# Kernel optimization log

Hardware: AMD Instinct MI355X
Metric: run time of the kernel (lower is better)

The kernel has to match this reference:

```python
import jax, jax.numpy as jnp
import numpy as np

EPS = 1e-5
THRESH = 0.05
NUM_THINGS = 3
D = 256
EGO_PC_RANGE = np.array([-51.2, -51.2, -5.0, 51.2, 51.2, 3.0], np.float32)


def _inverse_sigmoid(x):
    x = jnp.clip(x, 0.0, 1.0)
    return jnp.log(jnp.maximum(x, EPS) / jnp.maximum(1.0 - x, EPS))


def setup_inputs() -> dict:
    key = jax.random.key(0)
    ks = jax.random.split(key, 16)
    L, B, Qo, Qv = 6, 1, 8192, 8192
    # class logits uniform in [0,1) -> sigmoid >= 0.5 > threshold, so all queries pass (deterministic shapes)
    other_outputs_classes = jax.random.uniform(ks[0], (L, B, Qo, NUM_THINGS), jnp.float32)
    other_outputs_coords = jax.random.uniform(ks[1], (L, B, Qo, 4), jnp.float32)
    other_query = jax.random.normal(ks[2], (B, Qo, D), jnp.float32)
    other_query_pos = jax.random.normal(ks[3], (B, Qo, D), jnp.float32)
    other_reference = jax.random.normal(ks[4], (B, Qo, 4), jnp.float32)
    veh_outputs_classes = jax.random.normal(ks[5], (L, B, Qv, NUM_THINGS), jnp.float32)
    veh_outputs_coords = jax.random.uniform(ks[6], (L, B, Qv, 4), jnp.float32)
    veh_query = jax.random.normal(ks[7], (B, Qv, D), jnp.float32)
    veh_query_pos = jax.random.normal(ks[8], (B, Qv, D), jnp.float32)
    veh_reference = jax.random.normal(ks[9], (B, Qv, 4), jnp.float32)
    # rigid ego->other transform (rotation about z + translation), invertible by construction
    th = 0.3
    rt = np.eye(4, dtype=np.float32)
    rt[0, 0] = np.cos(th); rt[0, 1] = -np.sin(th)
    rt[1, 0] = np.sin(th); rt[1, 1] = np.cos(th)
    rt[0, 3] = 12.0; rt[1, 3] = -5.0; rt[2, 3] = 0.3
    ego2other_rt = jnp.asarray(rt)[None]  # [1,4,4]
    other_agent_pc_range = jnp.asarray(EGO_PC_RANGE)
    xav = float(np.sqrt(2.0 / (D + 9 + D)))
    Wa = jax.random.normal(ks[10], (D + 9, D), jnp.float32) * xav
    ba = jax.random.normal(ks[11], (D,), jnp.float32) * 0.01
    Wp = jax.random.normal(ks[12], (D + 9, D), jnp.float32) * xav
    bp = jax.random.normal(ks[13], (D,), jnp.float32) * 0.01
    return dict(other_outputs_classes=other_outputs_classes, other_outputs_coords=other_outputs_coords,
                other_query=other_query, other_query_pos=other_query_pos, other_reference=other_reference,
                veh_outputs_classes=veh_outputs_classes, veh_outputs_coords=veh_outputs_coords,
                veh_query=veh_query, veh_query_pos=veh_query_pos, veh_reference=veh_reference,
                ego2other_rt=ego2other_rt, other_agent_pc_range=other_agent_pc_range,
                Wa=Wa, ba=ba, Wp=Wp, bp=bp)


def reference(other_outputs_classes, other_outputs_coords, other_query, other_query_pos, other_reference,
              veh_outputs_classes, veh_outputs_coords, veh_query, veh_query_pos, veh_reference,
              ego2other_rt, other_agent_pc_range, Wa, ba, Wp, bp):
    calib = jnp.linalg.inv(ego2other_rt[0].T)  # other -> ego, [4,4]
    # filter_other_lanes (eager: concrete inputs, data-dependent selection like torch.where)
    cls = jax.nn.sigmoid(other_outputs_classes[-1])
    bbox_index = jnp.where(cls.reshape(-1) > THRESH)[0] // NUM_THINGS
    ooc_cls = other_outputs_classes[:, :, bbox_index]      # [L,B,N,3]
    ooc = other_outputs_coords[:, :, bbox_index]           # [L,B,N,4]
    oq = other_query[:, bbox_index]                        # [B,N,D]
    oqp = other_query_pos[:, bbox_index]
    oref = other_reference[:, bbox_index]                  # [B,N,4]
    lo, hi = other_agent_pc_range[:3], other_agent_pc_range[3:]
    elo = jnp.asarray(EGO_PC_RANGE[:3]); ehi = jnp.asarray(EGO_PC_RANGE[3:])
    # --- reference points: inverse_sigmoid space, z logit = 0 ---
    p = jax.nn.sigmoid(jnp.concatenate([oref[..., :2], jnp.zeros_like(oref[..., :1])], -1))
    p = p * (hi - lo) + lo                                 # other lidar coords
    h = jnp.concatenate([p, jnp.ones_like(p[..., :1])], -1)
    p = jnp.einsum('ij,bnj->bni', calib, h)[..., :3]       # ego lidar coords
    p = _inverse_sigmoid((p - elo) / (ehi - elo))
    oref = jnp.concatenate([p[..., :2], oref[..., 2:]], -1)
    # --- bbox centers: already sigmoided, z norm = 0 ---
    b = jnp.concatenate([ooc[..., :2], jnp.zeros_like(ooc[..., :1])], -1)
    b = b * (hi - lo) + lo
    hb = jnp.concatenate([b, jnp.ones_like(b[..., :1])], -1)
    b = jnp.einsum('ij,lbnj->lbni', calib, hb)[..., :3]
    b = (b - elo) / (ehi - elo)
    ooc = jnp.concatenate([b[..., :2], ooc[..., 2:]], -1)
    # --- cross-agent query alignment: concat flattened 3x3 rotation, small Linear ---
    r9 = jnp.broadcast_to(calib[:3, :3].reshape(9), oq.shape[:2] + (9,))
    oq = jnp.concatenate([oq, r9], -1) @ Wa + ba
    oqp = jnp.concatenate([oqp, r9], -1) @ Wp + bp
    return (jnp.concatenate([veh_outputs_classes, ooc_cls], axis=2),
            jnp.concatenate([veh_outputs_coords, ooc], axis=2),
            jnp.concatenate([veh_query, oq], axis=1),
            jnp.concatenate([veh_query_pos, oqp], axis=1),
            jnp.concatenate([veh_reference, oref], axis=1))
```

## Files before the change

kernel.cpp:

```cpp
#include <hip/hip_runtime.h>
#include <stdint.h>

typedef float f32x4 __attribute__((ext_vector_type(4)));
typedef __bf16 bf16x8 __attribute__((ext_vector_type(8)));
typedef __bf16 bf16x4 __attribute__((ext_vector_type(4)));

namespace {
constexpr int L = 6, Qo = 8192, Qv = 8192, NT = 3, D = 256;
constexpr int ROWS = Qv + 3 * Qo;
constexpr int OUT0 = 0;
constexpr int OUT1 = L * ROWS * NT;
constexpr int OUT2 = OUT1 + L * ROWS * 4;
constexpr int OUT3 = OUT2 + ROWS * D;
constexpr int OUT4 = OUT3 + ROWS * D;
constexpr float ELO0 = -51.2f, ELO1 = -51.2f, EHI0 = 51.2f, EHI1 = 51.2f;
constexpr int NB_GEMM = 512;
constexpr int NB_STREAM = 1536;
constexpr int NB_TOT = NB_GEMM + NB_STREAM;
constexpr int R_COPY = 2 * Qv * D / 4;
constexpr int R_OUT1 = R_COPY + L * ROWS;
constexpr int R_OUT4 = R_OUT1 + ROWS;
constexpr int R_TOT  = R_OUT4 + L * ROWS * NT / 4;
}

__device__ __forceinline__ float sigmoidf(float x) { return 1.f / (1.f + __expf(-x)); }
__device__ __forceinline__ float invsig(float v) {
    float x = fminf(fmaxf(v, 0.f), 1.f);
    return __logf(fmaxf(x, 1e-5f) / fmaxf(1.f - x, 1e-5f));
}

__device__ void inv4x4_T(const float* __restrict__ rt, float* __restrict__ C) {
    float m[16], inv[16];
    for (int i = 0; i < 4; i++)
        for (int j = 0; j < 4; j++) m[i * 4 + j] = rt[j * 4 + i];
    inv[0]  =  m[5]*m[10]*m[15] - m[5]*m[11]*m[14] - m[9]*m[6]*m[15] + m[9]*m[7]*m[14] + m[13]*m[6]*m[11] - m[13]*m[7]*m[10];
    inv[4]  = -m[4]*m[10]*m[15] + m[4]*m[11]*m[14] + m[8]*m[6]*m[15] - m[8]*m[7]*m[14] - m[12]*m[6]*m[11] + m[12]*m[7]*m[10];
    inv[8]  =  m[4]*m[9]*m[15]  - m[4]*m[11]*m[13] - m[8]*m[5]*m[15] + m[8]*m[7]*m[13] + m[12]*m[5]*m[11] - m[12]*m[7]*m[9];
    inv[12] = -m[4]*m[9]*m[14]  + m[4]*m[10]*m[13] + m[8]*m[5]*m[14] - m[8]*m[6]*m[13] - m[12]*m[5]*m[10] + m[12]*m[6]*m[9];
    inv[1]  = -m[1]*m[10]*m[15] + m[1]*m[11]*m[14] + m[9]*m[2]*m[15] - m[9]*m[3]*m[14] - m[13]*m[2]*m[11] + m[13]*m[3]*m[10];
    inv[5]  =  m[0]*m[10]*m[15] - m[0]*m[11]*m[14] - m[8]*m[2]*m[15] + m[8]*m[3]*m[14] + m[12]*m[2]*m[11] - m[12]*m[3]*m[10];
    inv[9]  = -m[0]*m[9]*m[15]  + m[0]*m[11]*m[13] + m[8]*m[1]*m[15] - m[8]*m[3]*m[13] - m[12]*m[1]*m[11] + m[12]*m[3]*m[9];
    inv[13] =  m[0]*m[9]*m[14]  - m[0]*m[10]*m[13] - m[8]*m[1]*m[14] + m[8]*m[2]*m[13] + m[12]*m[1]*m[10] - m[12]*m[2]*m[9];
    inv[2]  =  m[1]*m[6]*m[15]  - m[1]*m[7]*m[14]  - m[5]*m[2]*m[15] + m[5]*m[3]*m[14] + m[13]*m[2]*m[7]  - m[13]*m[3]*m[6];
    inv[6]  = -m[0]*m[6]*m[15]  + m[0]*m[7]*m[14]  + m[4]*m[2]*m[15] - m[4]*m[3]*m[14] - m[12]*m[2]*m[7]  + m[12]*m[3]*m[6];
    inv[10] =  m[0]*m[5]*m[15]  - m[0]*m[7]*m[13]  - m[4]*m[1]*m[15] + m[4]*m[3]*m[13] + m[12]*m[1]*m[7]  - m[12]*m[3]*m[5];
    inv[14] = -m[0]*m[5]*m[14]  + m[0]*m[6]*m[13]  + m[4]*m[1]*m[14] - m[4]*m[2]*m[13] - m[12]*m[1]*m[6]  + m[12]*m[2]*m[5];
    inv[3]  = -m[1]*m[6]*m[11]  + m[1]*m[7]*m[10]  + m[5]*m[2]*m[11] - m[5]*m[3]*m[10] - m[9]*m[2]*m[7]   + m[9]*m[3]*m[6];
    inv[7]  =  m[0]*m[6]*m[11]  - m[0]*m[7]*m[10]  - m[4]*m[2]*m[11] + m[4]*m[3]*m[10] + m[8]*m[2]*m[7]   - m[8]*m[3]*m[6];
    inv[11] = -m[0]*m[5]*m[11]  + m[0]*m[7]*m[9]   + m[4]*m[1]*m[11] - m[4]*m[3]*m[9]  - m[8]*m[1]*m[7]   + m[8]*m[3]*m[5];
    inv[15] =  m[0]*m[5]*m[10]  - m[0]*m[6]*m[9]   - m[4]*m[1]*m[10] + m[4]*m[2]*m[9]  + m[8]*m[1]*m[6]   - m[8]*m[2]*m[5];
    float det = m[0]*inv[0] + m[1]*inv[4] + m[2]*inv[8] + m[3]*inv[12];
    det = 1.0f / det;
    for (int i = 0; i < 16; i++) C[i] = inv[i] * det;
}

__global__ __launch_bounds__(256, 8) void fused(
    const float* __restrict__ ocls, const float* __restrict__ ocoord,
    const float* __restrict__ oq, const float* __restrict__ oqp,
    const float* __restrict__ oref, const float* __restrict__ vcls,
    const float* __restrict__ vcoord, const float* __restrict__ vq,
    const float* __restrict__ vqp, const float* __restrict__ vref,
    const float* __restrict__ rt, const float* __restrict__ pcr,
    const float* __restrict__ Wa, const float* __restrict__ ba,
    const float* __restrict__ Wp, const float* __restrict__ bp,
    float* __restrict__ out) {
    __shared__ __attribute__((aligned(16))) char lds[16576];
    float* ldsBias  = (float*)&lds[16384];
    float* ldsCalib = (float*)&lds[16512];
    const int b = blockIdx.x;
    const int t = threadIdx.x;

    if (b < NB_GEMM) {
        const int r = b & 7, ny = (b >> 3) & 7, s = b >> 6;
        const int u = s * 8 + r, which = u >> 5, mg = u & 31;
        const float* Asrc = which ? oqp : oq;
        const float* Wsrc = which ? Wp : Wa;
        const float* bv   = which ? bp : ba;
        const size_t obase = which ? (size_t)OUT3 : (size_t)OUT2;
        const int n0 = ny * 32;
        if (t == 0) inv4x4_T(rt, ldsCalib);
        {
            int kloc = t >> 3;
            int n4 = (t & 7) * 4;
            #pragma unroll
            for (int pass = 0; pass < 8; ++pass) {
                int k = pass * 32 + kloc;
                f32x4 v = *(const f32x4*)&Wsrc[(size_t)k * D + n0 + n4];
                #pragma unroll
                for (int i = 0; i < 4; ++i) {
                    int n = n4 + i;
                    *(__bf16*)&lds[n * 512 + ((2 * k) ^ ((n & 7) << 4))] = (__bf16)v[i];
                }
            }
        }
        __syncthreads();
        if (t < 32) {
            float sum = bv[n0 + t];
            #pragma unroll
            for (int m2 = 0; m2 < 9; m2++)
                sum += ldsCalib[(m2 / 3) * 4 + (m2 % 3)] * Wsrc[(size_t)(D + m2) * D + n0 + t];
            ldsBias[t] = sum;
        }
        __syncthreads();
        const int lane = t & 63, wave = t >> 6, lrow = lane & 15, grp = lane >> 4;
        #pragma unroll
        for (int mi = 0; mi < 4; ++mi) {
            const int am = (mg * 4 + mi) * 64 + wave * 16 + lrow;
            const float* Ap = Asrc + (size_t)am * D;
            f32x4 acc[2] = {f32x4{0,0,0,0}, f32x4{0,0,0,0}};
            #pragma unroll
            for (int ks = 0; ks < 8; ++ks) {
                f32x4 a0 = *(const f32x4*)&Ap[ks * 32 + grp * 8];
                f32x4 a1 = *(const f32x4*)&Ap[ks * 32 + grp * 8 + 4];
                bf16x8 af = {(__bf16)a0.x, (__bf16)a0.y, (__bf16)a0.z, (__bf16)a0.w,
                             (__bf16)a1.x, (__bf16)a1.y, (__bf16)a1.z, (__bf16)a1.w};
                int kb = ks * 64 + grp * 16;
                #pragma unroll
                for (int nt = 0; nt < 2; ++nt) {
                    int c = nt * 16 + lrow;
                    bf16x8 w = *(const bf16x8*)&lds[c * 512 + (kb ^ ((c & 7) << 4))];
                    acc[nt] = __builtin_amdgcn_mfma_f32_16x16x32_bf16(w, af, acc[nt], 0, 0, 0);
                }
            }
            size_t rbase = obase + (size_t)(Qv + 3 * am) * D + n0;
            #pragma unroll
            for (int nt = 0; nt < 2; ++nt) {
                f32x4 bz = *(const f32x4*)&ldsBias[nt * 16 + grp * 4];
                f32x4 v = acc[nt] + bz;
                float* p = out + rbase + nt * 16 + grp * 4;
                *(f32x4*)p = v;
                *(f32x4*)(p + D) = v;
                *(f32x4*)(p + 2 * D) = v;
            }
        }
        return;
    }

    if (t == 0) inv4x4_T(rt, ldsCalib);
    __syncthreads();
    const float c00 = ldsCalib[0], c01 = ldsCalib[1], c02 = ldsCalib[2], c03 = ldsCalib[3];
    const float c10 = ldsCalib[4], c11 = ldsCalib[5], c12 = ldsCalib[6], c13 = ldsCalib[7];
    const float lo0 = pcr[0], lo1 = pcr[1], lo2 = pcr[2];
    const float hi0 = pcr[3], hi1 = pcr[4], hi2 = pcr[5];
    const int stride = NB_STREAM * 256;
    for (int c = (b - NB_GEMM) * 256 + t; c < R_TOT; c += stride) {
        if (c < R_COPY) {
            const int HALF = Qv * D / 4;
            const float* src = (c < HALF) ? vq : vqp;
            size_t ob = (c < HALF) ? (size_t)OUT2 : (size_t)OUT3;
            int j = (c < HALF) ? c : c - HALF;
            *(f32x4*)&out[ob + (size_t)j * 4] = *(const f32x4*)&src[(size_t)j * 4];
        } else if (c < R_OUT1) {
            int tid = c - R_COPY;
            unsigned l = (unsigned)tid >> 15, rr = (unsigned)tid & 32767u;
            f32x4 o;
            if (rr < (unsigned)Qv) {
                o = *(const f32x4*)&vcoord[((size_t)l * Qv + rr) * 4];
            } else {
                unsigned q = (rr - Qv) / 3u;
                f32x4 s = *(const f32x4*)&ocoord[((size_t)l * Qo + q) * 4];
                float bx = s.x * (hi0 - lo0) + lo0;
                float by = s.y * (hi1 - lo1) + lo1;
                float bz = lo2;
                float px = c00 * bx + c01 * by + c02 * bz + c03;
                float py = c10 * bx + c11 * by + c12 * bz + c13;
                o.x = (px - ELO0) / (EHI0 - ELO0);
                o.y = (py - ELO1) / (EHI1 - ELO1);
                o.z = s.z; o.w = s.w;
            }
            *(f32x4*)&out[OUT1 + (size_t)tid * 4] = o;
        } else if (c < R_OUT4) {
            unsigned rr = (unsigned)(c - R_OUT1);
            f32x4 o;
            if (rr < (unsigned)Qv) {
                o = *(const f32x4*)&vref[(size_t)rr * 4];
            } else {
                unsigned q = (rr - Qv) / 3u;
                f32x4 s = *(const f32x4*)&oref[(size_t)q * 4];
                float bx = sigmoidf(s.x) * (hi0 - lo0) + lo0;
                float by = sigmoidf(s.y) * (hi1 - lo1) + lo1;
                float bz = 0.5f * (hi2 - lo2) + lo2;
                float px = c00 * bx + c01 * by + c02 * bz + c03;
                float py = c10 * bx + c11 * by + c12 * bz + c13;
                o.x = invsig((px - ELO0) / (EHI0 - ELO0));
                o.y = invsig((py - ELO1) / (EHI1 - ELO1));
                o.z = s.z; o.w = s.w;
            }
            *(f32x4*)&out[OUT4 + (size_t)rr * 4] = o;
        } else {
            int e0 = (c - R_OUT4) * 4;
            f32x4 o;
            #pragma unroll
            for (int i = 0; i < 4; ++i) {
                unsigned e = (unsigned)(e0 + i);
                unsigned l = e / (unsigned)(ROWS * NT);
                unsigned rem = e - l * (ROWS * NT);
                unsigned rr = rem / 3u;
                float v;
                if (rr < (unsigned)Qv) v = vcls[l * (Qv * NT) + rem];
                else {
                    unsigned cc = rem - rr * 3u;
                    unsigned q = (rr - Qv) / 3u;
                    v = ocls[l * (Qo * NT) + q * 3u + cc];
                }
                o[i] = v;
            }
            *(f32x4*)&out[OUT0 + (size_t)e0] = o;
        }
    }
}

extern "C" void kernel_launch(void* const* d_in, const int* in_sizes, int n_in,
                              void* d_out, int out_size, void* d_ws, size_t ws_size,
                              hipStream_t stream) {
    const float* ocls   = (const float*)d_in[0];
    const float* ocoord = (const float*)d_in[1];
    const float* oq     = (const float*)d_in[2];
    const float* oqp    = (const float*)d_in[3];
    const float* oref   = (const float*)d_in[4];
    const float* vcls   = (const float*)d_in[5];
    const float* vcoord = (const float*)d_in[6];
    const float* vq     = (const float*)d_in[7];
    const float* vqp    = (const float*)d_in[8];
    const float* vref   = (const float*)d_in[9];
    const float* rt     = (const float*)d_in[10];
    const float* pcr    = (const float*)d_in[11];
    const float* Wa     = (const float*)d_in[12];
    const float* ba     = (const float*)d_in[13];
    const float* Wp     = (const float*)d_in[14];
    const float* bp     = (const float*)d_in[15];
    float* out = (float*)d_out;

    hipLaunchKernelGGL(fused, dim3(NB_TOT), dim3(256), 0, stream,
                       ocls, ocoord, oq, oqp, oref, vcls, vcoord, vq, vqp, vref,
                       rt, pcr, Wa, ba, Wp, bp, out);
}
```

Measured before the change: 30.89 us.

## Split fused kernel into separate GEMM and streaming-copy launches with finer work split

Replaces the single fused kernel, which gave GEMM blocks and grid-strided stream blocks role-based work, with two kernels. The GEMM kernel now launches 2048 blocks that each handle one 64-row M tile instead of four. The stream kernel uses a fixed, non-strided mapping of 1024 vec4 elements per block, with separate block ranges for the plain copies, the coord/ref transforms and the class gather. The aim is better load balance and fewer branches per thread, at the cost of a second launch and no overlap between GEMM and streaming work. Each GEMM block also redoes the weight-tile staging and matrix inverse for less work.

```diff
diff --git a/kernel.cpp b/kernel.cpp
--- a/kernel.cpp
+++ b/kernel.cpp
@@ -14,13 +14,13 @@
 constexpr int OUT3 = OUT2 + ROWS * D;
 constexpr int OUT4 = OUT3 + ROWS * D;
 constexpr float ELO0 = -51.2f, ELO1 = -51.2f, EHI0 = 51.2f, EHI1 = 51.2f;
-constexpr int NB_GEMM = 512;
-constexpr int NB_STREAM = 1536;
-constexpr int NB_TOT = NB_GEMM + NB_STREAM;
+constexpr int NB_GEMM = 2048;
 constexpr int R_COPY = 2 * Qv * D / 4;
 constexpr int R_OUT1 = R_COPY + L * ROWS;
 constexpr int R_OUT4 = R_OUT1 + ROWS;
 constexpr int R_TOT  = R_OUT4 + L * ROWS * NT / 4;
+constexpr int NB_STREAM = R_TOT / 1024;
+constexpr int HALF = Qv * D / 4;
 }
 
 __device__ __forceinline__ float sigmoidf(float x) { return 1.f / (1.f + __expf(-x)); }
@@ -54,159 +54,171 @@
     for (int i = 0; i < 16; i++) C[i] = inv[i] * det;
 }
 
-__global__ __launch_bounds__(256, 8) void fused(
+__global__ __launch_bounds__(256, 8) void k_gemm(
+    const float* __restrict__ oq, const float* __restrict__ oqp,
+    const float* __restrict__ Wa, const float* __restrict__ ba,
+    const float* __restrict__ Wp, const float* __restrict__ bp,
+    const float* __restrict__ rt, float* __restrict__ out) {
+    __shared__ __attribute__((aligned(16))) char lds[16576];
+    float* ldsBias  = (float*)&lds[16384];
+    float* ldsCalib = (float*)&lds[16512];
+    const int b = blockIdx.x, t = threadIdx.x;
+    const int ny = b >> 8, mg = (b & 255) >> 1, which = b & 1;
+    const float* Asrc = which ? oqp : oq;
+    const float* Wsrc = which ? Wp : Wa;
+    const float* bv   = which ? bp : ba;
+    const size_t obase = which ? (size_t)OUT3 : (size_t)OUT2;
+    const int n0 = ny * 32;
+    if (t == 0) inv4x4_T(rt, ldsCalib);
+    {
+        int kloc = t >> 3;
+        int n4 = (t & 7) * 4;
+        #pragma unroll
+        for (int pass = 0; pass < 8; ++pass) {
+            int k = pass * 32 + kloc;
+            f32x4 v = *(const f32x4*)&Wsrc[(size_t)k * D + n0 + n4];
+            #pragma unroll
+            for (int i = 0; i < 4; ++i) {
+                int n = n4 + i;
+                *(__bf16*)&lds[n * 512 + ((2 * k) ^ ((n & 7) << 4))] = (__bf16)v[i];
+            }
+        }
+    }
+    __syncthreads();
+    if (t < 32) {
+        float sum = bv[n0 + t];
+        #pragma unroll
+        for (int m2 = 0; m2 < 9; m2++)
+            sum += ldsCalib[(m2 / 3) * 4 + (m2 % 3)] * Wsrc[(size_t)(D + m2) * D + n0 + t];
+        ldsBias[t] = sum;
+    }
+    __syncthreads();
+    const int lane = t & 63, wave = t >> 6, lrow = lane & 15, grp = lane >> 4;
+    const int am = mg * 64 + wave * 16 + lrow;
+    const float* Ap = Asrc + (size_t)am * D;
+    f32x4 acc[2] = {f32x4{0,0,0,0}, f32x4{0,0,0,0}};
+    #pragma unroll
+    for (int ks = 0; ks < 8; ++ks) {
+        f32x4 a0 = *(const f32x4*)&Ap[ks * 32 + grp * 8];
+        f32x4 a1 = *(const f32x4*)&Ap[ks * 32 + grp * 8 + 4];
+        bf16x8 af = {(__bf16)a0.x, (__bf16)a0.y, (__bf16)a0.z, (__bf16)a0.w,
+                     (__bf16)a1.x, (__bf16)a1.y, (__bf16)a1.z, (__bf16)a1.w};
+        int kb = ks * 64 + grp * 16;
+        #pragma unroll
+        for (int nt = 0; nt < 2; ++nt) {
+            int c = nt * 16 + lrow;
+            bf16x8 w = *(const bf16x8*)&lds[c * 512 + (kb ^ ((c & 7) << 4))];
+            acc[nt] = __builtin_amdgcn_mfma_f32_16x16x32_bf16(w, af, acc[nt], 0, 0, 0);
+        }
+    }
+    size_t rbase = obase + (size_t)(Qv + 3 * am) * D + n0;
+    #pragma unroll
+    for (int nt = 0; nt < 2; ++nt) {
+        f32x4 bz = *(const f32x4*)&ldsBias[nt * 16 + grp * 4];
+        f32x4 v = acc[nt] + bz;
+        float* p = out + rbase + nt * 16 + grp * 4;
+        *(f32x4*)p = v;
+        *(f32x4*)(p + D) = v;
+        *(f32x4*)(p + 2 * D) = v;
+    }
+}
+
+__global__ __launch_bounds__(256, 8) void k_stream(
     const float* __restrict__ ocls, const float* __restrict__ ocoord,
-    const float* __restrict__ oq, const float* __restrict__ oqp,
     const float* __restrict__ oref, const float* __restrict__ vcls,
     const float* __restrict__ vcoord, const float* __restrict__ vq,
     const float* __restrict__ vqp, const float* __restrict__ vref,
     const float* __restrict__ rt, const float* __restrict__ pcr,
-    const float* __restrict__ Wa, const float* __restrict__ ba,
-    const float* __restrict__ Wp, const float* __restrict__ bp,
     float* __restrict__ out) {
-    __shared__ __attribute__((aligned(16))) char lds[16576];
-    float* ldsBias  = (float*)&lds[16384];
-    float* ldsCalib = (float*)&lds[16512];
-    const int b = blockIdx.x;
-    const int t = threadIdx.x;
-
-    if (b < NB_GEMM) {
-        const int r = b & 7, ny = (b >> 3) & 7, s = b >> 6;
-        const int u = s * 8 + r, which = u >> 5, mg = u & 31;
-        const float* Asrc = which ? oqp : oq;
-        const float* Wsrc = which ? Wp : Wa;
-        const float* bv   = which ? bp : ba;
-        const size_t obase = which ? (size_t)OUT3 : (size_t)OUT2;
-        const int n0 = ny * 32;
+    __shared__ float ldsCalib[16];
+    const int b = blockIdx.x, t = threadIdx.x;
+
+    if (b < 1024) {
+        const float* src = (b < 512) ? vq : vqp;
+        const size_t ob = (b < 512) ? (size_t)OUT2 : (size_t)OUT3;
+        const int j0 = (b & 511) * 1024 + t;
+        f32x4 v0 = *(const f32x4*)&src[(size_t)j0 * 4];
+        f32x4 v1 = *(const f32x4*)&src[(size_t)(j0 + 256) * 4];
+        f32x4 v2 = *(const f32x4*)&src[(size_t)(j0 + 512) * 4];
+        f32x4 v3 = *(const f32x4*)&src[(size_t)(j0 + 768) * 4];
+        *(f32x4*)&out[ob + (size_t)j0 * 4] = v0;
+        *(f32x4*)&out[ob + (size_t)(j0 + 256) * 4] = v1;
+        *(f32x4*)&out[ob + (size_t)(j0 + 512) * 4] = v2;
+        *(f32x4*)&out[ob + (size_t)(j0 + 768) * 4] = v3;
+        return;
+    }
+    if (b < 1248) {
         if (t == 0) inv4x4_T(rt, ldsCalib);
-        {
-            int kloc = t >> 3;
-            int n4 = (t & 7) * 4;
-            #pragma unroll
-            for (int pass = 0; pass < 8; ++pass) {
-                int k = pass * 32 + kloc;
-                f32x4 v = *(const f32x4*)&Wsrc[(size_t)k * D + n0 + n4];
-                #pragma unroll
-                for (int i = 0; i < 4; ++i) {
-                    int n = n4 + i;
-                    *(__bf16*)&lds[n * 512 + ((2 * k) ^ ((n & 7) << 4))] = (__bf16)v[i];
+        __syncthreads();
+        const float c00 = ldsCalib[0], c01 = ldsCalib[1], c02 = ldsCalib[2], c03 = ldsCalib[3];
+        const float c10 = ldsCalib[4], c11 = ldsCalib[5], c12 = ldsCalib[6], c13 = ldsCalib[7];
+        const float lo0 = pcr[0], lo1 = pcr[1], lo2 = pcr[2];
+        const float hi0 = pcr[3], hi1 = pcr[4], hi2 = pcr[5];
+        #pragma unroll
+        for (int k = 0; k < 4; ++k) {
+            int c = b * 1024 + t + k * 256;
+            if (c < R_OUT1) {
+                int tid = c - R_COPY;
+                unsigned l = (unsigned)tid >> 15, rr = (unsigned)tid & 32767u;
+                f32x4 o;
+                if (rr < (unsigned)Qv) {
+                    o = *(const f32x4*)&vcoord[((size_t)l * Qv + rr) * 4];
+                } else {
+                    unsigned q = (rr - Qv) / 3u;
+                    f32x4 s = *(const f32x4*)&ocoord[((size_t)l * Qo + q) * 4];
+                    float bx = s.x * (hi0 - lo0) + lo0;
+                    float by = s.y * (hi1 - lo1) + lo1;
+                    float bz = lo2;
+                    float px = c00 * bx + c01 * by + c02 * bz + c03;
+                    float py = c10 * bx + c11 * by + c12 * bz + c13;
+                    o.x = (px - ELO0) / (EHI0 - ELO0);
+                    o.y = (py - ELO1) / (EHI1 - ELO1);
+                    o.z = s.z; o.w = s.w;
                 }
+                *(f32x4*)&out[OUT1 + (size_t)tid * 4] = o;
+            } else {
+                unsigned rr = (unsigned)(c - R_OUT1);
+                f32x4 o;
+                if (rr < (unsigned)Qv) {
+                    o = *(const f32x4*)&vref[(size_t)rr * 4];
+                } else {
+                    unsigned q = (rr - Qv) / 3u;
+                    f32x4 s = *(const f32x4*)&oref[(size_t)q * 4];
+                    float bx = sigmoidf(s.x) * (hi0 - lo0) + lo0;
+                    float by = sigmoidf(s.y) * (hi1 - lo1) + lo1;
+                    float bz = 0.5f * (hi2 - lo2) + lo2;
+                    float px = c00 * bx + c01 * by + c02 * bz + c03;
+                    float py = c10 * bx + c11 * by + c12 * bz + c13;
+                    o.x = invsig((px - ELO0) / (EHI0 - ELO0));
+                    o.y = invsig((py - ELO1) / (EHI1 - ELO1));
+                    o.z = s.z; o.w = s.w;
+                }
+                *(f32x4*)&out[OUT4 + (size_t)rr * 4] = o;
             }
         }
-        __syncthreads();
-        if (t < 32) {
-            float sum = bv[n0 + t];
-            #pragma unroll
-            for (int m2 = 0; m2 < 9; m2++)
-                sum += ldsCalib[(m2 / 3) * 4 + (m2 % 3)] * Wsrc[(size_t)(D + m2) * D + n0 + t];
-            ldsBias[t] = sum;
-        }
-        __syncthreads();
-        const int lane = t & 63, wave = t >> 6, lrow = lane & 15, grp = lane >> 4;
-        #pragma unroll
-        for (int mi = 0; mi < 4; ++mi) {
-            const int am = (mg * 4 + mi) * 64 + wave * 16 + lrow;
-            const float* Ap = Asrc + (size_t)am * D;
-            f32x4 acc[2] = {f32x4{0,0,0,0}, f32x4{0,0,0,0}};
-            #pragma unroll
-            for (int ks = 0; ks < 8; ++ks) {
-                f32x4 a0 = *(const f32x4*)&Ap[ks * 32 + grp * 8];
-                f32x4 a1 = *(const f32x4*)&Ap[ks * 32 + grp * 8 + 4];
-                bf16x8 af = {(__bf16)a0.x, (__bf16)a0.y, (__bf16)a0.z, (__bf16)a0.w,
-                             (__bf16)a1.x, (__bf16)a1.y, (__bf16)a1.z, (__bf16)a1.w};
-                int kb = ks * 64 + grp * 16;
-                #pragma unroll
-                for (int nt = 0; nt < 2; ++nt) {
-                    int c = nt * 16 + lrow;
-                    bf16x8 w = *(const bf16x8*)&lds[c * 512 + (kb ^ ((c & 7) << 4))];
-                    acc[nt] = __builtin_amdgcn_mfma_f32_16x16x32_bf16(w, af, acc[nt], 0, 0, 0);
-                }
+        return;
+    }
+    #pragma unroll
+    for (int k = 0; k < 4; ++k) {
+        int c = b * 1024 + t + k * 256;
+        int e0 = (c - R_OUT4) * 4;
+        f32x4 o;
+        #pragma unroll
+        for (int i = 0; i < 4; ++i) {
+            unsigned e = (unsigned)(e0 + i);
+            unsigned l = e / (unsigned)(ROWS * NT);
+            unsigned rem = e - l * (ROWS * NT);
+            unsigned rr = rem / 3u;
+            float v;
+            if (rr < (unsigned)Qv) v = vcls[l * (Qv * NT) + rem];
+            else {
+                unsigned cc = rem - rr * 3u;
+                unsigned q = (rr - Qv) / 3u;
+                v = ocls[l * (Qo * NT) + q * 3u + cc];
             }
-            size_t rbase = obase + (size_t)(Qv + 3 * am) * D + n0;
-            #pragma unroll
-            for (int nt = 0; nt < 2; ++nt) {
-                f32x4 bz = *(const f32x4*)&ldsBias[nt * 16 + grp * 4];
-                f32x4 v = acc[nt] + bz;
-                float* p = out + rbase + nt * 16 + grp * 4;
-                *(f32x4*)p = v;
-                *(f32x4*)(p + D) = v;
-                *(f32x4*)(p + 2 * D) = v;
-            }
-        }
-        return;
-    }
-
-    if (t == 0) inv4x4_T(rt, ldsCalib);
-    __syncthreads();
-    const float c00 = ldsCalib[0], c01 = ldsCalib[1], c02 = ldsCalib[2], c03 = ldsCalib[3];
-    const float c10 = ldsCalib[4], c11 = ldsCalib[5], c12 = ldsCalib[6], c13 = ldsCalib[7];
-    const float lo0 = pcr[0], lo1 = pcr[1], lo2 = pcr[2];
-    const float hi0 = pcr[3], hi1 = pcr[4], hi2 = pcr[5];
-    const int stride = NB_STREAM * 256;
-    for (int c = (b - NB_GEMM) * 256 + t; c < R_TOT; c += stride) {
-        if (c < R_COPY) {
-            const int HALF = Qv * D / 4;
-            const float* src = (c < HALF) ? vq : vqp;
-            size_t ob = (c < HALF) ? (size_t)OUT2 : (size_t)OUT3;
-            int j = (c < HALF) ? c : c - HALF;
-            *(f32x4*)&out[ob + (size_t)j * 4] = *(const f32x4*)&src[(size_t)j * 4];
-        } else if (c < R_OUT1) {
-            int tid = c - R_COPY;
-            unsigned l = (unsigned)tid >> 15, rr = (unsigned)tid & 32767u;
-            f32x4 o;
-            if (rr < (unsigned)Qv) {
-                o = *(const f32x4*)&vcoord[((size_t)l * Qv + rr) * 4];
-            } else {
-                unsigned q = (rr - Qv) / 3u;
-                f32x4 s = *(const f32x4*)&ocoord[((size_t)l * Qo + q) * 4];
-                float bx = s.x * (hi0 - lo0) + lo0;
-                float by = s.y * (hi1 - lo1) + lo1;
-                float bz = lo2;
-                float px = c00 * bx + c01 * by + c02 * bz + c03;
-                float py = c10 * bx + c11 * by + c12 * bz + c13;
-                o.x = (px - ELO0) / (EHI0 - ELO0);
-                o.y = (py - ELO1) / (EHI1 - ELO1);
-                o.z = s.z; o.w = s.w;
-            }
-            *(f32x4*)&out[OUT1 + (size_t)tid * 4] = o;
-        } else if (c < R_OUT4) {
-            unsigned rr = (unsigned)(c - R_OUT1);
-            f32x4 o;
-            if (rr < (unsigned)Qv) {
-                o = *(const f32x4*)&vref[(size_t)rr * 4];
-            } else {
-                unsigned q = (rr - Qv) / 3u;
-                f32x4 s = *(const f32x4*)&oref[(size_t)q * 4];
-                float bx = sigmoidf(s.x) * (hi0 - lo0) + lo0;
-                float by = sigmoidf(s.y) * (hi1 - lo1) + lo1;
-                float bz = 0.5f * (hi2 - lo2) + lo2;
-                float px = c00 * bx + c01 * by + c02 * bz + c03;
-                float py = c10 * bx + c11 * by + c12 * bz + c13;
-                o.x = invsig((px - ELO0) / (EHI0 - ELO0));
-                o.y = invsig((py - ELO1) / (EHI1 - ELO1));
-                o.z = s.z; o.w = s.w;
-            }
-            *(f32x4*)&out[OUT4 + (size_t)rr * 4] = o;
-        } else {
-            int e0 = (c - R_OUT4) * 4;
-            f32x4 o;
-            #pragma unroll
-            for (int i = 0; i < 4; ++i) {
-                unsigned e = (unsigned)(e0 + i);
-                unsigned l = e / (unsigned)(ROWS * NT);
-                unsigned rem = e - l * (ROWS * NT);
-                unsigned rr = rem / 3u;
-                float v;
-                if (rr < (unsigned)Qv) v = vcls[l * (Qv * NT) + rem];
-                else {
-                    unsigned cc = rem - rr * 3u;
-                    unsigned q = (rr - Qv) / 3u;
-                    v = ocls[l * (Qo * NT) + q * 3u + cc];
-                }
-                o[i] = v;
-            }
-            *(f32x4*)&out[OUT0 + (size_t)e0] = o;
-        }
+            o[i] = v;
+        }
+        *(f32x4*)&out[OUT0 + (size_t)e0] = o;
     }
 }
 
@@ -231,7 +243,8 @@
     const float* bp     = (const float*)d_in[15];
     float* out = (float*)d_out;
 
-    hipLaunchKernelGGL(fused, dim3(NB_TOT), dim3(256), 0, stream,
-                       ocls, ocoord, oq, oqp, oref, vcls, vcoord, vq, vqp, vref,
-                       rt, pcr, Wa, ba, Wp, bp, out);
-}
+    hipLaunchKernelGGL(k_gemm, dim3(NB_GEMM), dim3(256), 0, stream,
+                       oq, oqp, Wa, ba, Wp, bp, rt, out);
+    hipLaunchKernelGGL(k_stream, dim3(NB_STREAM), dim3(256), 0, stream,
+                       ocls, ocoord, oref, vcls, vcoord, vq, vqp, vref, rt, pcr, out);
+}
```

After: 37.88 us. 22.6% more time.

## Stage A tile through LDS with coalesced loads in fused GEMM blocks

Applied to the files above, without the earlier changes.

The GEMM blocks now load each 64-row A tile cooperatively with coalesced row-contiguous reads, convert it to bf16 and store it in a swizzled LDS region, then feed the MFMAs from LDS instead of strided per-lane global loads. LDS per block grows from about 16KB to about 48KB and the occupancy hint in launch_bounds is removed. Two extra barriers per m-tile and the mi loop is no longer unrolled. The larger LDS use lowers occupancy, which may hurt the streaming blocks that share the same kernel.

```diff
diff --git a/kernel.cpp b/kernel.cpp
--- a/kernel.cpp
+++ b/kernel.cpp
@@ -17,6 +17,9 @@
 constexpr int NB_GEMM = 512;
 constexpr int NB_STREAM = 1536;
 constexpr int NB_TOT = NB_GEMM + NB_STREAM;
+constexpr int LDSA = 16384;
+constexpr int LDSBIAS = LDSA + 32768;
+constexpr int LDSCAL = LDSBIAS + 128;
 constexpr int R_COPY = 2 * Qv * D / 4;
 constexpr int R_OUT1 = R_COPY + L * ROWS;
 constexpr int R_OUT4 = R_OUT1 + ROWS;
@@ -54,7 +57,7 @@
     for (int i = 0; i < 16; i++) C[i] = inv[i] * det;
 }
 
-__global__ __launch_bounds__(256, 8) void fused(
+__global__ __launch_bounds__(256) void fused(
     const float* __restrict__ ocls, const float* __restrict__ ocoord,
     const float* __restrict__ oq, const float* __restrict__ oqp,
     const float* __restrict__ oref, const float* __restrict__ vcls,
@@ -64,9 +67,9 @@
     const float* __restrict__ Wa, const float* __restrict__ ba,
     const float* __restrict__ Wp, const float* __restrict__ bp,
     float* __restrict__ out) {
-    __shared__ __attribute__((aligned(16))) char lds[16576];
-    float* ldsBias  = (float*)&lds[16384];
-    float* ldsCalib = (float*)&lds[16512];
+    __shared__ __attribute__((aligned(16))) char lds[49344];
+    float* ldsBias  = (float*)&lds[LDSBIAS];
+    float* ldsCalib = (float*)&lds[LDSCAL];
     const int b = blockIdx.x;
     const int t = threadIdx.x;
 
@@ -103,18 +106,29 @@
         }
         __syncthreads();
         const int lane = t & 63, wave = t >> 6, lrow = lane & 15, grp = lane >> 4;
-        #pragma unroll
         for (int mi = 0; mi < 4; ++mi) {
-            const int am = (mg * 4 + mi) * 64 + wave * 16 + lrow;
-            const float* Ap = Asrc + (size_t)am * D;
+            const float* Abase = Asrc + (size_t)(mg * 4 + mi) * 64 * D;
+            #pragma unroll
+            for (int i = 0; i < 8; ++i) {
+                int flat = i * 256 + t;
+                int row = flat >> 5;
+                int cu8 = flat & 31;
+                const float* src = Abase + (size_t)row * D + cu8 * 8;
+                f32x4 a0 = *(const f32x4*)src;
+                f32x4 a1 = *(const f32x4*)(src + 4);
+                bf16x8 w = {(__bf16)a0.x, (__bf16)a0.y, (__bf16)a0.z, (__bf16)a0.w,
+                            (__bf16)a1.x, (__bf16)a1.y, (__bf16)a1.z, (__bf16)a1.w};
+                *(bf16x8*)&lds[LDSA + row * 512 + ((cu8 * 16) ^ ((row & 7) << 4))] = w;
+            }
+            __syncthreads();
+            const int arow = wave * 16 + lrow;
+            const int abase = LDSA + arow * 512;
+            const int aswz = (lrow & 7) << 4;
             f32x4 acc[2] = {f32x4{0,0,0,0}, f32x4{0,0,0,0}};
             #pragma unroll
             for (int ks = 0; ks < 8; ++ks) {
-                f32x4 a0 = *(const f32x4*)&Ap[ks * 32 + grp * 8];
-                f32x4 a1 = *(const f32x4*)&Ap[ks * 32 + grp * 8 + 4];
-                bf16x8 af = {(__bf16)a0.x, (__bf16)a0.y, (__bf16)a0.z, (__bf16)a0.w,
-                             (__bf16)a1.x, (__bf16)a1.y, (__bf16)a1.z, (__bf16)a1.w};
                 int kb = ks * 64 + grp * 16;
+                bf16x8 af = *(const bf16x8*)&lds[abase + (kb ^ aswz)];
                 #pragma unroll
                 for (int nt = 0; nt < 2; ++nt) {
                     int c = nt * 16 + lrow;
@@ -122,6 +136,8 @@
                     acc[nt] = __builtin_amdgcn_mfma_f32_16x16x32_bf16(w, af, acc[nt], 0, 0, 0);
                 }
             }
+            __syncthreads();
+            const int am = (mg * 4 + mi) * 64 + arow;
             size_t rbase = obase + (size_t)(Qv + 3 * am) * D + n0;
             #pragma unroll
             for (int nt = 0; nt < 2; ++nt) {
@@ -148,8 +164,8 @@
             const int HALF = Qv * D / 4;
             const float* src = (c < HALF) ? vq : vqp;
             size_t ob = (c < HALF) ? (size_t)OUT2 : (size_t)OUT3;
-            int j = (c < HALF) ? c : c - HALF;
-            *(f32x4*)&out[ob + (size_t)j * 4] = *(const f32x4*)&src[(size_t)j * 4];
+            int jj = (c < HALF) ? c : c - HALF;
+            *(f32x4*)&out[ob + (size_t)jj * 4] = *(const f32x4*)&src[(size_t)jj * 4];
         } else if (c < R_OUT1) {
             int tid = c - R_COPY;
             unsigned l = (unsigned)tid >> 15, rr = (unsigned)tid & 32767u;
```

Result: faster. 27.46 us (-11.1%).
